# Performance work log

Measured on AMD Instinct MI355X. Metric: run time of the kernel, lower is better.

Reference implementation:

```python
import jax, jax.numpy as jnp
import numpy as np

SEQ_LEN = 768
PRED_LEN = 192
ENC_IN = 321
BATCH = 2
N_ORDER = 256
MULTISCALE = (1, 2, 4)
MODES = 32  # min(32, min(pred_len, seq_len)//2)


def _transition(N):
    Q = np.arange(N, dtype=np.float64)
    R = (2 * Q + 1)[:, None]
    j, i = np.meshgrid(Q, Q)
    A = np.where(i < j, -1, (-1.0) ** (i - j + 1)) * R
    B = (-1.0) ** Q[:, None] * R
    return A, B


def _hippo_legt(N, dt):
    # bilinear (Tustin) discretization, identical to scipy.signal.cont2discrete(..., method='bilinear')
    A, Bc = _transition(N)
    I = np.eye(N)
    M = I - (dt / 2.0) * A
    Ad = np.linalg.solve(M, I + (dt / 2.0) * A)
    Bd = np.linalg.solve(M, dt * Bc)[:, 0]
    # eval_matrix: Legendre P_n(1 - 2*vals), vals = arange(0, 1, dt)
    vals = np.arange(0.0, 1.0, dt)
    x = 1.0 - 2.0 * vals
    P = np.zeros((len(vals), N))
    P[:, 0] = 1.0
    if N > 1:
        P[:, 1] = x
    for n in range(1, N - 1):
        P[:, n + 1] = ((2 * n + 1) * x * P[:, n] - n * P[:, n - 1]) / (n + 1)
    return Ad.astype(np.float32), Bd.astype(np.float32), P.astype(np.float32)


def setup_inputs() -> dict:
    key = jax.random.key(0)
    k = jax.random.split(key, 6)
    A_l, B_l, E_l = [], [], []
    for ms in MULTISCALE:
        Ad, Bd, E = _hippo_legt(N_ORDER, 1.0 / PRED_LEN / ms)
        A_l.append(Ad); B_l.append(Bd); E_l.append(jnp.asarray(E))
    scale = 1.0 / (N_ORDER * N_ORDER)
    return {
        "history_data": jax.random.normal(k[0], (BATCH, SEQ_LEN, ENC_IN, 1), jnp.float32),
        "future_data": jax.random.normal(k[1], (BATCH, PRED_LEN, ENC_IN, 1), jnp.float32),
        "affine_weight": jnp.ones((1, 1, ENC_IN), jnp.float32),
        "affine_bias": jnp.zeros((1, 1, ENC_IN), jnp.float32),
        "A_stack": jnp.asarray(np.stack(A_l)),            # [3, N, N]
        "B_stack": jnp.asarray(np.stack(B_l)),            # [3, N]
        "E0": E_l[0], "E1": E_l[1], "E2": E_l[2],        # [ms*pred, N]
        "wr": scale * jax.random.uniform(k[2], (3, N_ORDER, N_ORDER, MODES), jnp.float32),
        "wi": scale * jax.random.uniform(k[3], (3, N_ORDER, N_ORDER, MODES), jnp.float32),
        "mlp_w": 0.3 * jax.random.normal(k[4], (1, 3), jnp.float32),
        "mlp_b": jnp.zeros((1,), jnp.float32),
        "batch_seen": 0, "epoch": 1, "train": 1,
    }


def _hippo_scan(x_in, A, Bv):
    # x_in: [B, Lw, H] -> states [Lw, B, H, N]
    inp = jnp.transpose(x_in, (1, 0, 2))  # [Lw, B, H]
    c0 = jnp.zeros(x_in.shape[:1] + x_in.shape[2:] + (A.shape[0],), x_in.dtype)  # [B, H, N]
    def step(c, f):
        c = c @ A.T + f[..., None] * Bv
        return c, c
    _, cs = jax.lax.scan(step, c0, inp)
    return cs


def _forward(history_data, affine_weight, affine_bias, A_stack, B_stack, evals, wr, wi, mlp_w, mlp_b):
    x_enc = history_data[:, :, :, 0]                      # [B, L, H]
    means = jax.lax.stop_gradient(jnp.mean(x_enc, axis=1, keepdims=True))
    x = x_enc - means
    stdev = jax.lax.stop_gradient(jnp.sqrt(jnp.mean(x * x, axis=1, keepdims=True) + 1e-5))
    x = x / stdev * affine_weight + affine_bias

    x_decs = []
    for i, ms in enumerate(MULTISCALE):
        Lw = ms * PRED_LEN
        x_in = x[:, -Lw:]                                  # [B, Lw, H]
        cs = _hippo_scan(x_in, A_stack[i], B_stack[i])     # [Lw, B, H, N]
        xc = jnp.transpose(cs, (1, 2, 3, 0))               # [B, H, N, Lw]
        # spectral conv: rfft -> complex mode mixing over N -> irfft
        xf = jnp.fft.rfft(xc)                              # [B, H, N, Lw//2+1]
        a = xf[..., :MODES]
        W = wr[i] + 1j * wi[i]                             # [N, N, MODES]
        of = jnp.einsum('bjix,iox->bjox', a, W)
        out_ft = jnp.pad(of, ((0, 0), (0, 0), (0, 0), (0, Lw // 2 + 1 - MODES)))
        o = jnp.fft.irfft(out_ft, n=Lw)                    # [B, H, N, Lw]
        x_dec_c = o[:, :, :, PRED_LEN - 1]                 # [B, H, N]
        x_dec = x_dec_c @ evals[i][-PRED_LEN:].T           # [B, H, pred]
        x_decs.append(x_dec)

    xd = jnp.stack(x_decs, axis=-1)                        # [B, H, pred, 3]
    xd = jnp.einsum('bhpk,k->bhp', xd, mlp_w[0]) + mlp_b[0]
    xd = jnp.transpose(xd, (0, 2, 1))                      # [B, pred, H]
    xd = (xd - affine_bias) / (affine_weight + 1e-10)
    xd = xd * stdev + means
    return xd[..., None]                                   # [B, pred, H, 1]


def reference(history_data, future_data, affine_weight, affine_bias, A_stack, B_stack, E0, E1, E2, wr, wi, mlp_w, mlp_b, batch_seen, epoch, train):
    return _forward(history_data, affine_weight, affine_bias, A_stack, B_stack, (E0, E1, E2), wr, wi, mlp_w, mlp_b)
```

## Files before the change

### kernel.cpp

```cpp
#include <hip/hip_runtime.h>

#define SEQ 768
#define PRED 192
#define ENC 321
#define NB 2
#define BE (NB*ENC)
#define CH 32

typedef float vf2 __attribute__((ext_vector_type(2)));
typedef short s4v __attribute__((ext_vector_type(4)));
typedef short s8v __attribute__((ext_vector_type(8)));
typedef float f32x4 __attribute__((ext_vector_type(4)));

union F4V2 { float4 f4; vf2 v2[2]; };
union S8U { s4v h[2]; s8v v; };

__device__ __forceinline__ float4 ldg4(const float* p) {
    return *reinterpret_cast<const float4*>(p);
}
__device__ __forceinline__ s8v ldg8s(const unsigned short* p) {
    return *reinterpret_cast<const s8v*>(p);
}
__device__ __forceinline__ void pklo(vf2& c, vf2 a, vf2 b) {
    asm("v_pk_fma_f32 %0, %1, %2, %0 op_sel:[0,0,0] op_sel_hi:[0,1,1]"
        : "+v"(c) : "v"(a), "v"(b));
}
__device__ __forceinline__ void pkhi(vf2& c, vf2 a, vf2 b) {
    asm("v_pk_fma_f32 %0, %1, %2, %0 op_sel:[1,0,0] op_sel_hi:[1,1,1]"
        : "+v"(c) : "v"(a), "v"(b));
}

__device__ __forceinline__ unsigned short f2bf(float f) {
    unsigned int u = __float_as_uint(f);
    u = (u + 0x7fffu + ((u >> 16) & 1u)) >> 16;
    return (unsigned short)u;
}
__device__ __forceinline__ float bf2f(unsigned short h) {
    return __uint_as_float(((unsigned int)h) << 16);
}

__host__ __device__ __forceinline__ int d_Lw(int s)    { return s==0?192:(s==1?384:768); }
__host__ __device__ __forceinline__ int d_Hoff(int s)  { return s==0?0:(s==1?49152:147456); }
__host__ __device__ __forceinline__ int d_twoff(int s) { return s==0?0:(s==1?6144:18432); }
__host__ __device__ __forceinline__ int d_Coff(int s)  { return s==0?0:(s==1?3145728:9437184); }
__host__ __device__ __forceinline__ int d_rowoff(int s){ return s==0?0:(s==1?192:576); }

__global__ void k_stats1(const float* __restrict__ hist,
                         float* __restrict__ ps, float* __restrict__ ps2) {
    int j  = blockIdx.x*64 + threadIdx.x;
    int b  = blockIdx.y;
    int z  = blockIdx.z;
    int ty = threadIdx.y;
    float s = 0.f, s2 = 0.f;
    if (j < ENC) {
        int t0 = z*96;
        for (int t = t0 + ty; t < t0 + 96; t += 4) {
            float v = hist[(size_t)b*SEQ*ENC + (size_t)t*ENC + j];
            s += v; s2 += v*v;
        }
    }
    __shared__ float l1[4][64], l2[4][64];
    l1[ty][threadIdx.x] = s; l2[ty][threadIdx.x] = s2;
    __syncthreads();
    if (ty == 0 && j < ENC) {
        float S  = l1[0][threadIdx.x]+l1[1][threadIdx.x]+l1[2][threadIdx.x]+l1[3][threadIdx.x];
        float S2 = l2[0][threadIdx.x]+l2[1][threadIdx.x]+l2[2][threadIdx.x]+l2[3][threadIdx.x];
        ps [((size_t)z*2 + b)*ENC + j] = S;
        ps2[((size_t)z*2 + b)*ENC + j] = S2;
    }
}

__global__ void k_stats2(const float* __restrict__ ps, const float* __restrict__ ps2,
                         float* __restrict__ meanb, float* __restrict__ stdb) {
    int i = blockIdx.x*256 + threadIdx.x;
    if (i >= BE) return;
    int b = i / ENC, j = i - b*ENC;
    float S = 0.f, S2 = 0.f;
    #pragma unroll
    for (int z = 0; z < 8; z++) {
        S  += ps [((size_t)z*2 + b)*ENC + j];
        S2 += ps2[((size_t)z*2 + b)*ENC + j];
    }
    float m   = S * (1.f/SEQ);
    float var = S2 * (1.f/SEQ) - m*m;
    meanb[b*ENC+j] = m;
    stdb[b*ENC+j]  = sqrtf(var + 1e-5f);
}

__global__ void k_norm(const float* __restrict__ hist,
                       const float* __restrict__ meanb, const float* __restrict__ stdb,
                       const float* __restrict__ aw, const float* __restrict__ ab,
                       float* __restrict__ xn) {
    int i = blockIdx.x*256 + threadIdx.x;
    if (i >= NB*SEQ*ENC) return;
    int j = i % ENC;
    int b = i / (SEQ*ENC);
    float v = (hist[i] - meanb[b*ENC+j]) / stdb[b*ENC+j];
    xn[i] = v * aw[j] + ab[j];
}

__global__ void k_tw(float2* __restrict__ twm, float2* __restrict__ gtm) {
    int i = blockIdx.x*256 + threadIdx.x;
    if (i >= 43008) return;
    int s, rem;
    if (i < 6144)       { s=0; rem=i; }
    else if (i < 18432) { s=1; rem=i-6144; }
    else                { s=2; rem=i-18432; }
    int Lw = d_Lw(s);
    int k = rem & 31, m = rem >> 5;
    const float TWO_PI = 6.28318530717958647692f;
    int km = (k*m) % Lw;
    float c, sn;
    sincosf(TWO_PI * km / Lw, &sn, &c);
    twm[i] = make_float2(c, -sn);
    int e = (k*(PRED-1-m)) % Lw; if (e < 0) e += Lw;
    float c2, s2v;
    sincosf(TWO_PI * e / Lw, &s2v, &c2);
    float coef = (k==0 ? 1.f : 2.f) / (float)Lw;
    gtm[i] = make_float2(coef*c2, coef*s2v);
}

__global__ void k_hinit(const float* __restrict__ Ast, const float* __restrict__ Bst,
                        float* __restrict__ apow, float* __restrict__ Hbuf) {
    int i = blockIdx.x*256 + threadIdx.x;
    if (i < 3*65536) apow[i] = Ast[i];
    if (i < 3*256) {
        int s = i >> 8, n = i & 255;
        Hbuf[d_Hoff(s) + n] = Bst[i];
    }
}

__device__ __forceinline__ void gemm32nt(float* As, float* Bs,
    const float* __restrict__ A, int Arows, const float* __restrict__ B,
    float* __restrict__ C, int m0, int n0)
{
    int tid = threadIdx.x;
    int tm = tid >> 4, tn = tid & 15;
    int lr = tid >> 3, lq = (tid & 7)*4;
    float a00=0.f,a01=0.f,a10=0.f,a11=0.f;
    for (int kt = 0; kt < 256; kt += 32) {
        __syncthreads();
        float4 fa = ldg4(A + (size_t)(m0+lr)*256 + kt + lq);
        float4 fb = ldg4(B + (size_t)(n0+lr)*256 + kt + lq);
        As[lr*33+lq]=fa.x; As[lr*33+lq+1]=fa.y; As[lr*33+lq+2]=fa.z; As[lr*33+lq+3]=fa.w;
        Bs[lr*33+lq]=fb.x; Bs[lr*33+lq+1]=fb.y; Bs[lr*33+lq+2]=fb.z; Bs[lr*33+lq+3]=fb.w;
        __syncthreads();
        #pragma unroll
        for (int q = 0; q < 32; q++) {
            float x0 = As[(tm*2)*33+q],  x1 = As[(tm*2+1)*33+q];
            float y0 = Bs[(tn*2)*33+q],  y1 = Bs[(tn*2+1)*33+q];
            a00 = fmaf(x0,y0,a00); a01 = fmaf(x0,y1,a01);
            a10 = fmaf(x1,y0,a10); a11 = fmaf(x1,y1,a11);
        }
    }
    int m = m0 + tm*2, n = n0 + tn*2;
    if (m < Arows)   { C[(size_t)m*256+n]     = a00; C[(size_t)m*256+n+1]     = a01; }
    if (m+1 < Arows) { C[(size_t)(m+1)*256+n] = a10; C[(size_t)(m+1)*256+n+1] = a11; }
}

__device__ __forceinline__ void gemm32nn(float* As, float* Bs,
    const float* __restrict__ A, const float* __restrict__ B,
    float* __restrict__ C, int m0, int n0)
{
    int tid = threadIdx.x;
    int tm = tid >> 4, tn = tid & 15;
    int lr = tid >> 3, lq = (tid & 7)*4;
    float a00=0.f,a01=0.f,a10=0.f,a11=0.f;
    for (int kt = 0; kt < 256; kt += 32) {
        __syncthreads();
        float4 fa = ldg4(A + (size_t)(m0+lr)*256 + kt + lq);
        float4 fb = ldg4(B + (size_t)(kt+lr)*256 + n0 + lq);
        As[lr*33+lq]=fa.x; As[lr*33+lq+1]=fa.y; As[lr*33+lq+2]=fa.z; As[lr*33+lq+3]=fa.w;
        Bs[lr*33+lq]=fb.x; Bs[lr*33+lq+1]=fb.y; Bs[lr*33+lq+2]=fb.z; Bs[lr*33+lq+3]=fb.w;
        __syncthreads();
        #pragma unroll
        for (int q = 0; q < 32; q++) {
            float x0 = As[(tm*2)*33+q], x1 = As[(tm*2+1)*33+q];
            float y0 = Bs[q*33+tn*2],   y1 = Bs[q*33+tn*2+1];
            a00 = fmaf(x0,y0,a00); a01 = fmaf(x0,y1,a01);
            a10 = fmaf(x1,y0,a10); a11 = fmaf(x1,y1,a11);
        }
    }
    int m = m0 + tm*2, n = n0 + tn*2;
    C[(size_t)m*256+n]     = a00; C[(size_t)m*256+n+1]     = a01;
    C[(size_t)(m+1)*256+n] = a10; C[(size_t)(m+1)*256+n+1] = a11;
}

__global__ void __launch_bounds__(256) k_hlevel32(float* __restrict__ Hbuf,
                                                  float* __restrict__ apow,
                                                  int par, int mc) {
    __shared__ float As[32*33];
    __shared__ float Bs[32*33];
    int s = blockIdx.z;
    int Lw = d_Lw(s);
    const float* Asrc = apow + (size_t)par*196608 + (size_t)s*65536;
    float* Adst       = apow + (size_t)(1-par)*196608 + (size_t)s*65536;
    float* H = Hbuf + d_Hoff(s);
    int yt = blockIdx.y, xt = blockIdx.x;
    if (yt < 8) {
        if (mc >= Lw) return;
        int rows = min(mc, Lw - mc);
        if (yt*32 >= rows) return;
        gemm32nt(As, Bs, H, rows, Asrc, H + (size_t)mc*256, yt*32, xt*32);
    } else {
        if (2*mc >= Lw) return;
        gemm32nn(As, Bs, Asrc, Asrc, Adst, (yt-8)*32, xt*32);
    }
}

__global__ void k_split_h(const float* __restrict__ Hbuf,
                          unsigned short* __restrict__ Hh,
                          unsigned short* __restrict__ Hl) {
    int i = blockIdx.x*256 + threadIdx.x;
    if (i >= 344064) return;
    int s, rem;
    if (i < 49152)       { s=0; rem=i; }
    else if (i < 147456) { s=1; rem=i-49152; }
    else                 { s=2; rem=i-147456; }
    int Lw = d_Lw(s);
    int row = rem >> 8, q = rem & 255;
    float f = Hbuf[i];
    unsigned short h = f2bf(f);
    float l = f - bf2f(h);
    size_t off = (size_t)d_Hoff(s) + (size_t)(q >> 5)*((size_t)Lw*32) + (size_t)row*32 + (q & 31);
    Hh[off] = h;
    Hl[off] = f2bf(l);
}

__global__ void __launch_bounds__(256) k_packb(
    const float* __restrict__ wr, const float* __restrict__ wi,
    unsigned short* __restrict__ Bph, unsigned short* __restrict__ Bpl)
{
    __shared__ float ldsq[128][36];
    int o  = blockIdx.x;
    int q0 = blockIdx.y*128;
    int s  = blockIdx.z;
    const float* wrS = wr + (size_t)s*2097152;
    const float* wiS = wi + (size_t)s*2097152;
    unsigned short* BphS = Bph + (size_t)s*4194304;
    unsigned short* BplS = Bpl + (size_t)s*4194304;
    int t  = threadIdx.x;
    int qr = t >> 1, half = (t & 1)*16;
    int kk = t & 31, qc = t >> 5;
    for (int c = 0; c < 2; c++) {
        const float* W = (c ? wiS : wrS) + (size_t)(q0+qr)*8192 + o*32 + half;
        float4 v0 = ldg4(W), v1 = ldg4(W+4), v2 = ldg4(W+8), v3 = ldg4(W+12);
        __syncthreads();
        *reinterpret_cast<float4*>(&ldsq[qr][half+0])  = v0;
        *reinterpret_cast<float4*>(&ldsq[qr][half+4])  = v1;
        *reinterpret_cast<float4*>(&ldsq[qr][half+8])  = v2;
        *reinterpret_cast<float4*>(&ldsq[qr][half+12]) = v3;
        __syncthreads();
        unsigned short hbuf[16], lbuf[16];
        #pragma unroll
        for (int j = 0; j < 16; j++) {
            float f = ldsq[qc*16 + j][kk];
            unsigned short h = f2bf(f);
            hbuf[j] = h;
            lbuf[j] = f2bf(f - bf2f(h));
        }
        int col = o*64 + kk*2 + c;
        int qb  = q0 + qc*16;
        size_t off = (size_t)(qb >> 5)*524288 + (size_t)col*32 + (qb & 31);
        #pragma unroll
        for (int j = 0; j < 2; j++) {
            *reinterpret_cast<s8v*>(BphS + off + j*8) = *reinterpret_cast<s8v*>(&hbuf[j*8]);
            *reinterpret_cast<s8v*>(BplS + off + j*8) = *reinterpret_cast<s8v*>(&lbuf[j*8]);
        }
    }
}

__device__ __forceinline__ s8v lds_frag(const short* s, int idx) {
    S8U u;
    u.h[0] = *reinterpret_cast<const s4v*>(s + idx);
    u.h[1] = *reinterpret_cast<const s4v*>(s + idx + 4);
    return u.v;
}

__global__ void __launch_bounds__(256) k_cgemm_mfma(
    const unsigned short* __restrict__ Hh, const unsigned short* __restrict__ Hl,
    const unsigned short* __restrict__ Bph, const unsigned short* __restrict__ Bpl,
    float* __restrict__ C)
{
    int t = threadIdx.x;
    int nwg = gridDim.x;
    int cpx = nwg >> 3;
    int bid = blockIdx.x;
    int lid = (bid & 7)*cpx + (bid >> 3);
    int s, local, mt;
    if (lid < 256)      { s = 0; local = lid;       mt = 2; }
    else if (lid < 640) { s = 1; local = lid - 256; mt = 3; }
    else                { s = 2; local = lid - 640; mt = 6; }
    int Lw = d_Lw(s);
    int bx = local % mt, by = local / mt;
    int m0 = bx*128, n0 = by*128;

    const unsigned short* HhS = Hh + d_Hoff(s);
    const unsigned short* HlS = Hl + d_Hoff(s);
    const unsigned short* BphS = Bph + (size_t)s*4194304;
    const unsigned short* BplS = Bpl + (size_t)s*4194304;
    float* CS = C + d_Coff(s);

    __shared__ short sA[2][128*36];
    __shared__ short sB[2][128*36];
    int lane = t & 63, wave = t >> 6;
    int wm = wave >> 1, wn = wave & 1;
    int srow = t >> 1, shalf = (t & 1)*16;
    size_t strideA = (size_t)Lw*32;
    size_t aRow = (size_t)(m0 + srow)*32 + shalf;
    size_t bRow = (size_t)(n0 + srow)*32 + shalf;
    int sOff = srow*36 + shalf;

    f32x4 acc[4][4];
    #pragma unroll
    for (int i = 0; i < 4; i++)
        #pragma unroll
        for (int j = 0; j < 4; j++)
            acc[i][j] = (f32x4){0.f, 0.f, 0.f, 0.f};

    S8U ah0, ah1, al0, al1, bh0, bh1, bl0, bl1;
    ah0.v = ldg8s(HhS + aRow);
    ah1.v = ldg8s(HhS + aRow + 8);
    al0.v = ldg8s(HlS + aRow);
    al1.v = ldg8s(HlS + aRow + 8);
    bh0.v = ldg8s(BphS + bRow);
    bh1.v = ldg8s(BphS + bRow + 8);
    bl0.v = ldg8s(BplS + bRow);
    bl1.v = ldg8s(BplS + bRow + 8);

    for (int kt = 0; kt < 256; kt += 32) {
        __syncthreads();
        *reinterpret_cast<s4v*>(&sA[0][sOff+0])  = ah0.h[0];
        *reinterpret_cast<s4v*>(&sA[0][sOff+4])  = ah0.h[1];
        *reinterpret_cast<s4v*>(&sA[0][sOff+8])  = ah1.h[0];
        *reinterpret_cast<s4v*>(&sA[0][sOff+12]) = ah1.h[1];
        *reinterpret_cast<s4v*>(&sA[1][sOff+0])  = al0.h[0];
        *reinterpret_cast<s4v*>(&sA[1][sOff+4])  = al0.h[1];
        *reinterpret_cast<s4v*>(&sA[1][sOff+8])  = al1.h[0];
        *reinterpret_cast<s4v*>(&sA[1][sOff+12]) = al1.h[1];
        *reinterpret_cast<s4v*>(&sB[0][sOff+0])  = bh0.h[0];
        *reinterpret_cast<s4v*>(&sB[0][sOff+4])  = bh0.h[1];
        *reinterpret_cast<s4v*>(&sB[0][sOff+8])  = bh1.h[0];
        *reinterpret_cast<s4v*>(&sB[0][sOff+12]) = bh1.h[1];
        *reinterpret_cast<s4v*>(&sB[1][sOff+0])  = bl0.h[0];
        *reinterpret_cast<s4v*>(&sB[1][sOff+4])  = bl0.h[1];
        *reinterpret_cast<s4v*>(&sB[1][sOff+8])  = bl1.h[0];
        *reinterpret_cast<s4v*>(&sB[1][sOff+12]) = bl1.h[1];
        __syncthreads();
        if (kt + 32 < 256) {
            int kb = (kt >> 5) + 1;
            ah0.v = ldg8s(HhS + kb*strideA + aRow);
            ah1.v = ldg8s(HhS + kb*strideA + aRow + 8);
            al0.v = ldg8s(HlS + kb*strideA + aRow);
            al1.v = ldg8s(HlS + kb*strideA + aRow + 8);
            bh0.v = ldg8s(BphS + (size_t)kb*524288 + bRow);
            bh1.v = ldg8s(BphS + (size_t)kb*524288 + bRow + 8);
            bl0.v = ldg8s(BplS + (size_t)kb*524288 + bRow);
            bl1.v = ldg8s(BplS + (size_t)kb*524288 + bRow + 8);
        }
        int klane = (lane >> 4) << 3;
        s8v Bfh[4], Bfl[4];
        #pragma unroll
        for (int tn = 0; tn < 4; tn++) {
            int cb = (wn*64 + tn*16 + (lane & 15))*36 + klane;
            Bfh[tn] = lds_frag(sB[0], cb);
            Bfl[tn] = lds_frag(sB[1], cb);
        }
        #pragma unroll
        for (int tm = 0; tm < 4; tm++) {
            int ca = (wm*64 + tm*16 + (lane & 15))*36 + klane;
            s8v Ah = lds_frag(sA[0], ca);
            s8v Al = lds_frag(sA[1], ca);
            #pragma unroll
            for (int tn = 0; tn < 4; tn++) {
                acc[tm][tn] = __builtin_amdgcn_mfma_f32_16x16x32_bf16(Ah, Bfh[tn], acc[tm][tn], 0, 0, 0);
                acc[tm][tn] = __builtin_amdgcn_mfma_f32_16x16x32_bf16(Ah, Bfl[tn], acc[tm][tn], 0, 0, 0);
                acc[tm][tn] = __builtin_amdgcn_mfma_f32_16x16x32_bf16(Al, Bfh[tn], acc[tm][tn], 0, 0, 0);
            }
        }
    }
    int r0 = (lane >> 4)*4, cc = lane & 15;
    #pragma unroll
    for (int tm = 0; tm < 4; tm++) {
        #pragma unroll
        for (int tn = 0; tn < 4; tn++) {
            int gcol = n0 + wn*64 + tn*16 + cc;
            int og = gcol >> 6, rem = gcol & 63;
            float* cp = CS + (size_t)og*((size_t)Lw*64) + rem;
            #pragma unroll
            for (int reg = 0; reg < 4; reg++) {
                int r = m0 + wm*64 + tm*16 + r0 + reg;
                if (r < Lw) cp[(size_t)r*64] = acc[tm][tn][reg];
            }
        }
    }
}

__global__ void k_cscan1(const float2* __restrict__ Call2, const float2* __restrict__ twm,
                         float2* __restrict__ psum) {
    int cg = blockIdx.x;
    int s  = (cg < 6) ? 0 : (cg < 18) ? 1 : 2;
    int cl = cg - ((s==0)?0:(s==1)?6:18);
    int Lw = d_Lw(s);
    int tid = threadIdx.x;
    int k = tid & 31, ol = tid >> 5;
    int o = blockIdx.y*8 + ol;
    const float2* tws = twm + d_twoff(s);
    const float2* Co = Call2 + (d_Coff(s) >> 1) + (size_t)o*((size_t)Lw*32);
    int mbase = cl*CH;
    float pr = 0.f, pi = 0.f;
    for (int mm = 0; mm < CH; mm++) {
        int m = mbase + mm;
        float2 cc = Co[(size_t)m*32 + k];
        float2 t  = tws[(size_t)m*32 + k];
        pr = fmaf(t.x, cc.x, pr); pr = fmaf(-t.y, cc.y, pr);
        pi = fmaf(t.x, cc.y, pi); pi = fmaf(t.y, cc.x, pi);
    }
    psum[((size_t)cg)*8192 + o*32 + k] = make_float2(pr, pi);
}

__global__ void k_cscan2(const float2* __restrict__ Call2, const float2* __restrict__ twm,
                         const float2* __restrict__ gtm, const float2* __restrict__ psum,
                         float* __restrict__ Qall) {
    int cg = blockIdx.x;
    int s  = (cg < 6) ? 0 : (cg < 18) ? 1 : 2;
    int cgbase = (s==0)?0:(s==1)?6:18;
    int cl = cg - cgbase;
    int Lw = d_Lw(s);
    float* Qrow = Qall + (size_t)d_rowoff(s)*256;
    int tid = threadIdx.x;
    int k = tid & 31, ol = tid >> 5;
    int o = blockIdx.y*8 + ol;
    const float2* tws = twm + d_twoff(s);
    const float2* gts = gtm + d_twoff(s);
    const float2* Co = Call2 + (d_Coff(s) >> 1) + (size_t)o*((size_t)Lw*32);
    float pr = 0.f, pi = 0.f;
    for (int c = 0; c < cl; c++) {
        float2 p = psum[((size_t)(cgbase+c))*8192 + o*32 + k];
        pr += p.x; pi += p.y;
    }
    int mbase = cl*CH;
    for (int mm = 0; mm < CH; mm++) {
        int m = mbase + mm;
        float2 cc = Co[(size_t)m*32 + k];
        float2 t  = tws[(size_t)m*32 + k];
        pr = fmaf(t.x, cc.x, pr); pr = fmaf(-t.y, cc.y, pr);
        pi = fmaf(t.x, cc.y, pi); pi = fmaf(t.y, cc.x, pi);
        int r = Lw - 1 - m;
        float2 g = gts[(size_t)r*32 + k];
        float qv = g.x*pr - g.y*pi;
        qv += __shfl_xor(qv, 16);
        qv += __shfl_xor(qv, 8);
        qv += __shfl_xor(qv, 4);
        qv += __shfl_xor(qv, 2);
        qv += __shfl_xor(qv, 1);
        if (k == 0) Qrow[(size_t)r*256 + o] = qv;
    }
}

__device__ __forceinline__ void gemm64nt(
    const float* __restrict__ A, int lda, int Arows,
    const float* __restrict__ B, int ldb,
    float* __restrict__ C, int ldc, int m0, int n0, int K)
{
    __shared__ __align__(16) float AsT[16][68];
    __shared__ __align__(16) float BsT[16][68];
    int tid = threadIdx.x;
    int tm = tid >> 4, tn = tid & 15;
    int lr = tid >> 2, lq = (tid & 3)*4;
    bool aok = (m0 + lr) < Arows;
    const float* Ap = A + (size_t)(m0+lr)*lda + lq;
    const float* Bp = B + (size_t)(n0+lr)*ldb + lq;
    float4 fa = aok ? ldg4(Ap) : make_float4(0.f,0.f,0.f,0.f);
    float4 fb = ldg4(Bp);
    vf2 acc[4][2] = {};
    for (int kt = 0; kt < K; kt += 16) {
        __syncthreads();
        AsT[lq+0][lr]=fa.x; AsT[lq+1][lr]=fa.y; AsT[lq+2][lr]=fa.z; AsT[lq+3][lr]=fa.w;
        BsT[lq+0][lr]=fb.x; BsT[lq+1][lr]=fb.y; BsT[lq+2][lr]=fb.z; BsT[lq+3][lr]=fb.w;
        __syncthreads();
        if (kt + 16 < K) {
            fa = aok ? ldg4(Ap + kt + 16) : make_float4(0.f,0.f,0.f,0.f);
            fb = ldg4(Bp + kt + 16);
        }
        #pragma unroll
        for (int q = 0; q < 16; q++) {
            F4V2 ua, ub;
            ua.f4 = *reinterpret_cast<float4*>(&AsT[q][tm*4]);
            ub.f4 = *reinterpret_cast<float4*>(&BsT[q][tn*4]);
            #pragma unroll
            for (int ra = 0; ra < 2; ra++)
                #pragma unroll
                for (int cp = 0; cp < 2; cp++) {
                    pklo(acc[2*ra+0][cp], ua.v2[ra], ub.v2[cp]);
                    pkhi(acc[2*ra+1][cp], ua.v2[ra], ub.v2[cp]);
                }
        }
    }
    #pragma unroll
    for (int r = 0; r < 4; r++) {
        int m = m0 + tm*4 + r; if (m >= Arows) continue;
        float4 o4 = make_float4(acc[r][0].x, acc[r][0].y, acc[r][1].x, acc[r][1].y);
        *reinterpret_cast<float4*>(C + (size_t)m*ldc + n0 + tn*4) = o4;
    }
}

__global__ void __launch_bounds__(256) k_tgemm(const float* __restrict__ Qall,
                                               const float* __restrict__ E0,
                                               const float* __restrict__ E1,
                                               const float* __restrict__ E2,
                                               float* __restrict__ T) {
    int mtg = blockIdx.x;
    int s, lm, Lw, rowoff, Toff;
    if (mtg < 3)      { s=0; lm=mtg;   Lw=192; rowoff=0;   Toff=0; }
    else if (mtg < 9) { s=1; lm=mtg-3; Lw=384; rowoff=192; Toff=36864; }
    else              { s=2; lm=mtg-9; Lw=768; rowoff=576; Toff=110592; }
    const float* Es = (s==0) ? E0 : ((s==1) ? E1 : E2);
    gemm64nt(Qall + (size_t)rowoff*256, 256, Lw,
             Es + (size_t)(Lw-192)*256, 256,
             T + Toff, 192, lm*64, blockIdx.y*64, 256);
}

__global__ void k_mtot(const float* __restrict__ T, const float* __restrict__ mlpw,
                       float* __restrict__ M) {
    int i = blockIdx.x*256 + threadIdx.x;
    if (i >= 192*768) return;
    int p = i / 768, t = i % 768;
    float v = mlpw[2] * T[110592 + (size_t)t*192 + p];
    if (t >= 384) v += mlpw[1] * T[36864 + (size_t)(t-384)*192 + p];
    if (t >= 576) v += mlpw[0] * T[(size_t)(t-576)*192 + p];
    M[i] = v;
}

__global__ void __launch_bounds__(256) k_finalA(
    const float* __restrict__ M, const float* __restrict__ xn,
    float* __restrict__ partial)
{
    __shared__ float Ms[4*128];
    int tid = threadIdx.x;
    int pg = blockIdx.y, z = blockIdx.z;
    #pragma unroll
    for (int e = tid; e < 512; e += 256) {
        int u = e >> 7, tt = e & 127;
        Ms[e] = M[(size_t)(pg*4 + u)*768 + z*128 + tt];
    }
    __syncthreads();
    int cc = blockIdx.x*256 + tid;
    if (cc >= BE) return;
    int b = (cc >= ENC) ? 1 : 0;
    int j = cc - b*ENC;
    const float* xp = xn + (size_t)b*SEQ*ENC + (size_t)(z*128)*ENC + j;
    float a0 = 0.f, a1 = 0.f, a2 = 0.f, a3 = 0.f;
    #pragma unroll 8
    for (int t = 0; t < 128; t++) {
        float xv = xp[(size_t)t*ENC];
        a0 = fmaf(Ms[t],       xv, a0);
        a1 = fmaf(Ms[128 + t], xv, a1);
        a2 = fmaf(Ms[256 + t], xv, a2);
        a3 = fmaf(Ms[384 + t], xv, a3);
    }
    size_t base = ((size_t)z*192 + pg*4)*BE + cc;
    partial[base]        = a0;
    partial[base + BE]   = a1;
    partial[base + 2*BE] = a2;
    partial[base + 3*BE] = a3;
}

__global__ void __launch_bounds__(256) k_finalB(
    const float* __restrict__ partial,
    const float* __restrict__ aw, const float* __restrict__ ab,
    const float* __restrict__ meanb, const float* __restrict__ stdb,
    const float* __restrict__ mlpb, float* __restrict__ out)
{
    int i = blockIdx.x*256 + threadIdx.x;
    if (i >= 192*BE) return;
    int p = i / BE, cc = i - p*BE;
    float s = 0.f;
    #pragma unroll
    for (int z = 0; z < 6; z++)
        s += partial[((size_t)z*192 + p)*BE + cc];
    int b = (cc >= ENC) ? 1 : 0;
    int j = cc - b*ENC;
    float v = (s + mlpb[0] - ab[j]) / (aw[j] + 1e-10f);
    v = v * stdb[b*ENC+j] + meanb[b*ENC+j];
    out[(size_t)b*(PRED*ENC) + (size_t)p*ENC + j] = v;
}

extern "C" void kernel_launch(void* const* d_in, const int* in_sizes, int n_in,
                              void* d_out, int out_size, void* d_ws, size_t ws_size,
                              hipStream_t stream)
{
    const float* hist = (const float*)d_in[0];
    const float* aw   = (const float*)d_in[2];
    const float* ab   = (const float*)d_in[3];
    const float* Ast  = (const float*)d_in[4];
    const float* Bst  = (const float*)d_in[5];
    const float* E0   = (const float*)d_in[6];
    const float* E1   = (const float*)d_in[7];
    const float* E2   = (const float*)d_in[8];
    const float* wr   = (const float*)d_in[9];
    const float* wi   = (const float*)d_in[10];
    const float* mlpw = (const float*)d_in[11];
    const float* mlpb = (const float*)d_in[12];
    float* out = (float*)d_out;

    float* w = (float*)d_ws;
    float* xn    = w; w += 493056;
    float* meanb = w; w += 642;
    float* stdb  = w; w += 642;
    float* pstat = w; w += 5136;
    float* pstat2= w; w += 5136;
    float* Hbuf  = w; w += 344064;
    float* apow  = w; w += 393216;
    float2* twm  = (float2*)w; w += 86016;
    float2* gtm  = (float2*)w; w += 86016;
    float2* psum = (float2*)w; w += 688128;
    unsigned short* Hh  = (unsigned short*)w; w += 172032;
    unsigned short* Hl  = (unsigned short*)w; w += 172032;
    unsigned short* Bph = (unsigned short*)w; w += 6291456;
    unsigned short* Bpl = (unsigned short*)w; w += 6291456;
    float* Call  = w; w += 22020096;
    float* Qall  = w; w += 344064;
    float* Tbuf  = w; w += 258048;
    float* Mt    = w; w += 147456;
    float* fpart = w; w += 739584;

    k_stats1<<<dim3(6,2,8), dim3(64,4), 0, stream>>>(hist, pstat, pstat2);
    k_stats2<<<3, 256, 0, stream>>>(pstat, pstat2, meanb, stdb);
    k_norm<<<1926, 256, 0, stream>>>(hist, meanb, stdb, aw, ab, xn);
    k_tw<<<168, 256, 0, stream>>>(twm, gtm);
    k_hinit<<<768, 256, 0, stream>>>(Ast, Bst, apow, Hbuf);
    for (int lev = 0; lev < 10; lev++)
        k_hlevel32<<<dim3(8,16,3), 256, 0, stream>>>(Hbuf, apow, lev & 1, 1 << lev);
    k_split_h<<<1344, 256, 0, stream>>>(Hbuf, Hh, Hl);
    k_packb<<<dim3(256,2,3), 256, 0, stream>>>(wr, wi, Bph, Bpl);

    k_cgemm_mfma<<<1408, 256, 0, stream>>>(Hh, Hl, Bph, Bpl, Call);
    k_cscan1<<<dim3(42, 32), 256, 0, stream>>>((const float2*)Call, twm, psum);
    k_cscan2<<<dim3(42, 32), 256, 0, stream>>>((const float2*)Call, twm, gtm, psum, Qall);

    k_tgemm<<<dim3(21,3), 256, 0, stream>>>(Qall, E0, E1, E2, Tbuf);
    k_mtot<<<576, 256, 0, stream>>>(Tbuf, mlpw, Mt);
    k_finalA<<<dim3(3, 48, 6), 256, 0, stream>>>(Mt, xn, fpart);
    k_finalB<<<482, 256, 0, stream>>>(fpart, aw, ab, meanb, stdb, mlpb, out);
}
```

Before: 278.4 us.

## Read Call once in chunked scan and add prefix correction separately; merge init kernels

The two-pass chunked prefix scan over Call (one pass computing chunk sums, a second rereading Call to form Q) is restructured. Each chunk now computes its local prefix and Q contribution in one pass and writes its chunk sum. A light fix-up kernel then adds the carried prefix times the g coefficients into Q, which works because Q is linear in the prefix. This removes one full read of the large Call buffer at the cost of a read-modify-write on Qall. Separately, the twiddle-init and hippo-init kernels are merged into a single launch.

```diff
diff --git a/kernel.cpp b/kernel.cpp
--- a/kernel.cpp
+++ b/kernel.cpp
@@ -99,34 +99,36 @@
     xn[i] = v * aw[j] + ab[j];
 }
 
-__global__ void k_tw(float2* __restrict__ twm, float2* __restrict__ gtm) {
-    int i = blockIdx.x*256 + threadIdx.x;
-    if (i >= 43008) return;
-    int s, rem;
-    if (i < 6144)       { s=0; rem=i; }
-    else if (i < 18432) { s=1; rem=i-6144; }
-    else                { s=2; rem=i-18432; }
-    int Lw = d_Lw(s);
-    int k = rem & 31, m = rem >> 5;
-    const float TWO_PI = 6.28318530717958647692f;
-    int km = (k*m) % Lw;
-    float c, sn;
-    sincosf(TWO_PI * km / Lw, &sn, &c);
-    twm[i] = make_float2(c, -sn);
-    int e = (k*(PRED-1-m)) % Lw; if (e < 0) e += Lw;
-    float c2, s2v;
-    sincosf(TWO_PI * e / Lw, &s2v, &c2);
-    float coef = (k==0 ? 1.f : 2.f) / (float)Lw;
-    gtm[i] = make_float2(coef*c2, coef*s2v);
-}
-
-__global__ void k_hinit(const float* __restrict__ Ast, const float* __restrict__ Bst,
-                        float* __restrict__ apow, float* __restrict__ Hbuf) {
-    int i = blockIdx.x*256 + threadIdx.x;
-    if (i < 3*65536) apow[i] = Ast[i];
-    if (i < 3*256) {
-        int s = i >> 8, n = i & 255;
-        Hbuf[d_Hoff(s) + n] = Bst[i];
+__global__ void k_init(float2* __restrict__ twm, float2* __restrict__ gtm,
+                       const float* __restrict__ Ast, const float* __restrict__ Bst,
+                       float* __restrict__ apow, float* __restrict__ Hbuf) {
+    int bid = blockIdx.x;
+    if (bid < 168) {
+        int i = bid*256 + threadIdx.x;
+        if (i >= 43008) return;
+        int s, rem;
+        if (i < 6144)       { s=0; rem=i; }
+        else if (i < 18432) { s=1; rem=i-6144; }
+        else                { s=2; rem=i-18432; }
+        int Lw = d_Lw(s);
+        int k = rem & 31, m = rem >> 5;
+        const float TWO_PI = 6.28318530717958647692f;
+        int km = (k*m) % Lw;
+        float c, sn;
+        sincosf(TWO_PI * km / Lw, &sn, &c);
+        twm[i] = make_float2(c, -sn);
+        int e = (k*(PRED-1-m)) % Lw; if (e < 0) e += Lw;
+        float c2, s2v;
+        sincosf(TWO_PI * e / Lw, &s2v, &c2);
+        float coef = (k==0 ? 1.f : 2.f) / (float)Lw;
+        gtm[i] = make_float2(coef*c2, coef*s2v);
+    } else {
+        int i = (bid-168)*256 + threadIdx.x;
+        if (i < 3*65536) apow[i] = Ast[i];
+        if (i < 3*256) {
+            int s = i >> 8, n = i & 255;
+            Hbuf[d_Hoff(s) + n] = Bst[i];
+        }
     }
 }
 
@@ -396,36 +398,12 @@
     }
 }
 
-__global__ void k_cscan1(const float2* __restrict__ Call2, const float2* __restrict__ twm,
-                         float2* __restrict__ psum) {
+__global__ void k_cscanF(const float2* __restrict__ Call2, const float2* __restrict__ twm,
+                         const float2* __restrict__ gtm, float2* __restrict__ psum,
+                         float* __restrict__ Qall) {
     int cg = blockIdx.x;
     int s  = (cg < 6) ? 0 : (cg < 18) ? 1 : 2;
     int cl = cg - ((s==0)?0:(s==1)?6:18);
-    int Lw = d_Lw(s);
-    int tid = threadIdx.x;
-    int k = tid & 31, ol = tid >> 5;
-    int o = blockIdx.y*8 + ol;
-    const float2* tws = twm + d_twoff(s);
-    const float2* Co = Call2 + (d_Coff(s) >> 1) + (size_t)o*((size_t)Lw*32);
-    int mbase = cl*CH;
-    float pr = 0.f, pi = 0.f;
-    for (int mm = 0; mm < CH; mm++) {
-        int m = mbase + mm;
-        float2 cc = Co[(size_t)m*32 + k];
-        float2 t  = tws[(size_t)m*32 + k];
-        pr = fmaf(t.x, cc.x, pr); pr = fmaf(-t.y, cc.y, pr);
-        pi = fmaf(t.x, cc.y, pi); pi = fmaf(t.y, cc.x, pi);
-    }
-    psum[((size_t)cg)*8192 + o*32 + k] = make_float2(pr, pi);
-}
-
-__global__ void k_cscan2(const float2* __restrict__ Call2, const float2* __restrict__ twm,
-                         const float2* __restrict__ gtm, const float2* __restrict__ psum,
-                         float* __restrict__ Qall) {
-    int cg = blockIdx.x;
-    int s  = (cg < 6) ? 0 : (cg < 18) ? 1 : 2;
-    int cgbase = (s==0)?0:(s==1)?6:18;
-    int cl = cg - cgbase;
     int Lw = d_Lw(s);
     float* Qrow = Qall + (size_t)d_rowoff(s)*256;
     int tid = threadIdx.x;
@@ -435,10 +413,6 @@
     const float2* gts = gtm + d_twoff(s);
     const float2* Co = Call2 + (d_Coff(s) >> 1) + (size_t)o*((size_t)Lw*32);
     float pr = 0.f, pi = 0.f;
-    for (int c = 0; c < cl; c++) {
-        float2 p = psum[((size_t)(cgbase+c))*8192 + o*32 + k];
-        pr += p.x; pi += p.y;
-    }
     int mbase = cl*CH;
     for (int mm = 0; mm < CH; mm++) {
         int m = mbase + mm;
@@ -455,6 +429,39 @@
         qv += __shfl_xor(qv, 2);
         qv += __shfl_xor(qv, 1);
         if (k == 0) Qrow[(size_t)r*256 + o] = qv;
+    }
+    psum[((size_t)cg)*8192 + o*32 + k] = make_float2(pr, pi);
+}
+
+__global__ void k_cfix(const float2* __restrict__ gtm, const float2* __restrict__ psum,
+                       float* __restrict__ Qall) {
+    int cg = blockIdx.x;
+    int s  = (cg < 6) ? 0 : (cg < 18) ? 1 : 2;
+    int cgbase = (s==0)?0:(s==1)?6:18;
+    int cl = cg - cgbase;
+    if (cl == 0) return;
+    int Lw = d_Lw(s);
+    float* Qrow = Qall + (size_t)d_rowoff(s)*256;
+    int tid = threadIdx.x;
+    int k = tid & 31, ol = tid >> 5;
+    int o = blockIdx.y*8 + ol;
+    const float2* gts = gtm + d_twoff(s);
+    float pr = 0.f, pi = 0.f;
+    for (int c = 0; c < cl; c++) {
+        float2 p = psum[((size_t)(cgbase+c))*8192 + o*32 + k];
+        pr += p.x; pi += p.y;
+    }
+    int mbase = cl*CH;
+    for (int mm = 0; mm < CH; mm++) {
+        int r = Lw - 1 - (mbase + mm);
+        float2 g = gts[(size_t)r*32 + k];
+        float qv = g.x*pr - g.y*pi;
+        qv += __shfl_xor(qv, 16);
+        qv += __shfl_xor(qv, 8);
+        qv += __shfl_xor(qv, 4);
+        qv += __shfl_xor(qv, 2);
+        qv += __shfl_xor(qv, 1);
+        if (k == 0) Qrow[(size_t)r*256 + o] += qv;
     }
 }
 
@@ -628,16 +635,15 @@
     k_stats1<<<dim3(6,2,8), dim3(64,4), 0, stream>>>(hist, pstat, pstat2);
     k_stats2<<<3, 256, 0, stream>>>(pstat, pstat2, meanb, stdb);
     k_norm<<<1926, 256, 0, stream>>>(hist, meanb, stdb, aw, ab, xn);
-    k_tw<<<168, 256, 0, stream>>>(twm, gtm);
-    k_hinit<<<768, 256, 0, stream>>>(Ast, Bst, apow, Hbuf);
+    k_init<<<936, 256, 0, stream>>>(twm, gtm, Ast, Bst, apow, Hbuf);
     for (int lev = 0; lev < 10; lev++)
         k_hlevel32<<<dim3(8,16,3), 256, 0, stream>>>(Hbuf, apow, lev & 1, 1 << lev);
     k_split_h<<<1344, 256, 0, stream>>>(Hbuf, Hh, Hl);
     k_packb<<<dim3(256,2,3), 256, 0, stream>>>(wr, wi, Bph, Bpl);
 
     k_cgemm_mfma<<<1408, 256, 0, stream>>>(Hh, Hl, Bph, Bpl, Call);
-    k_cscan1<<<dim3(42, 32), 256, 0, stream>>>((const float2*)Call, twm, psum);
-    k_cscan2<<<dim3(42, 32), 256, 0, stream>>>((const float2*)Call, twm, gtm, psum, Qall);
+    k_cscanF<<<dim3(42, 32), 256, 0, stream>>>((const float2*)Call, twm, gtm, psum, Qall);
+    k_cfix<<<dim3(42, 32), 256, 0, stream>>>(gtm, psum, Qall);
 
     k_tgemm<<<dim3(21,3), 256, 0, stream>>>(Qall, E0, E1, E2, Tbuf);
     k_mtot<<<576, 256, 0, stream>>>(Tbuf, mlpw, Mt);
```

After: 282.1 us. No clear change (+1.3%).
